# Performance work log

Measured on AMD Instinct MI355X. Metric: run time of the kernel, lower is better.

Reference implementation:

```python
import jax, jax.numpy as jnp
import numpy as np

DIM = 256
L = 16            # block_size (query rows per leaf block)
H = 8             # num_heads
D = DIM // H      # head_dim = 32
KC = L + 1        # key count: L leaf nodes + 1 block (mean) node, layout '16x17'
B = 2
N = 32768         # multiple of L -> no padding path
NB = N // L       # 2048 blocks
SCALE = D ** -0.5


def setup_inputs() -> dict:
    key = jax.random.key(0)
    ks = jax.random.split(key, 8)
    x = jax.random.normal(ks[0], (B, N, DIM), jnp.float32)
    attn_mask = jax.random.randint(ks[1], (NB, L, KC), 0, 2, dtype=jnp.int32)
    ar = jnp.arange(L)
    attn_mask = attn_mask.at[:, ar, ar].set(1)  # self always visible -> no all-masked rows
    edge_feats = jax.random.normal(ks[2], (NB, L, KC, 4), jnp.float32)
    s = DIM ** -0.5
    Wqkv = jax.random.normal(ks[3], (3 * DIM, DIM), jnp.float32) * s
    bqkv = jnp.zeros((3 * DIM,), jnp.float32)
    Wproj = jax.random.normal(ks[4], (DIM, DIM), jnp.float32) * s
    bproj = jnp.zeros((DIM,), jnp.float32)
    Wgate = jax.random.normal(ks[5], (H, 4), jnp.float32) * 0.01  # nn.init.normal_(std=0.01)
    bgate = jnp.zeros((H,), jnp.float32)
    return {"x": x, "attn_mask": attn_mask, "edge_feats": edge_feats,
            "Wqkv": Wqkv, "bqkv": bqkv, "Wproj": Wproj, "bproj": bproj,
            "Wgate": Wgate, "bgate": bgate}


def reference(x, attn_mask, edge_feats, Wqkv, bqkv, Wproj, bproj, Wgate, bgate):
    # x: [B, N, C] -> blocks [B, NB, L, C]
    x_blk = x.reshape(B, NB, L, DIM)
    block_node = x_blk.mean(axis=2, keepdims=True)           # virtual block node
    kv = jnp.concatenate([x_blk, block_node], axis=2)         # [B, NB, KC, C]

    # qkv projections (slice of the fused Linear; rows are independent so math is identical)
    q = x_blk @ Wqkv[:DIM].T + bqkv[:DIM]
    k = kv @ Wqkv[DIM:2 * DIM].T + bqkv[DIM:2 * DIM]
    v = kv @ Wqkv[2 * DIM:].T + bqkv[2 * DIM:]
    q = q.reshape(B, NB, L, H, D)
    k = k.reshape(B, NB, KC, H, D)
    v = v.reshape(B, NB, KC, H, D)

    scores = jnp.einsum('bnqhd,bnkhd->bnqkh', q, k) * SCALE   # [B, NB, L, KC, H]

    # physics bias: zero out + set channel 3 = 1 for block node column and self (diagonal)
    ar = jnp.arange(L)
    unit = jnp.array([0.0, 0.0, 0.0, 1.0], edge_feats.dtype)
    bias = edge_feats.at[:, :, L, :].set(unit)                # block-node column
    bias = bias.at[:, ar, ar, :].set(unit)                    # self bias on diagonal
    bias = jnp.broadcast_to(bias[None], (B, NB, L, KC, 4))    # expand over batch

    scores = scores + bias[..., 3:4]

    mask0 = (attn_mask[None] == 0)[..., None]                 # [1, NB, L, KC, 1]
    scores = jnp.where(mask0, -jnp.inf, scores)
    attn = jax.nn.softmax(scores, axis=3)

    gate = jnp.einsum('bnqkf,hf->bnqkh', bias, Wgate) + bgate  # edge-conditioned gate
    gate = jnp.where(mask0, 0.0, gate)

    combined = attn + gate
    out = jnp.einsum('bnqkh,bnkhd->bnqhd', combined, v).reshape(B, N, DIM)
    return out @ Wproj.T + bproj
```

## Files before the change

### kernel.cpp

```cpp
#include <hip/hip_runtime.h>
#include <cstdint>
#include <cstddef>

#define B_SZ 2
#define N_SEQ 32768
#define NB 2048
#define HD 32
#define LQ 16
#define KCNT 17
#define M_ROWS 65536
#define SCALE_F 0.17677669529663687f

typedef __attribute__((ext_vector_type(8))) short sv8;
typedef __attribute__((ext_vector_type(4))) short sv4;
typedef __attribute__((ext_vector_type(4))) float f4;

__device__ __forceinline__ short f2bf(float f) {
  unsigned u = __builtin_bit_cast(unsigned, f);
  u = (u + 0x7FFFu + ((u >> 16) & 1u)) >> 16;
  return (short)u;
}
__device__ __forceinline__ float bf2f(short s) {
  unsigned u = ((unsigned)(unsigned short)s) << 16;
  return __builtin_bit_cast(float, u);
}
__device__ __forceinline__ void gload16(const void* g, void* l) {
  __builtin_amdgcn_global_load_lds(
      (const __attribute__((address_space(1))) unsigned int*)g,
      (__attribute__((address_space(3))) unsigned int*)l, 16, 0, 0);
}
__device__ __forceinline__ f4 mfma16(sv8 a, sv8 b, f4 c) {
  return __builtin_amdgcn_mfma_f32_16x16x32_bf16(a, b, c, 0, 0, 0);
}

__global__ __launch_bounds__(256) void split256(const float* __restrict__ src,
                                                short* __restrict__ dst, int n4) {
  int i = blockIdx.x * 256 + threadIdx.x;
  if (i >= n4) return;
  float4 v = ((const float4*)src)[i];
  size_t row = (size_t)(i >> 6);
  int c = (i & 63) * 4;
  float fv[4] = {v.x, v.y, v.z, v.w};
  sv4 hi, lo;
#pragma unroll
  for (int j = 0; j < 4; ++j) {
    short h = f2bf(fv[j]);
    hi[j] = h;
    lo[j] = f2bf(fv[j] - bf2f(h));
  }
  *(sv4*)&dst[row * 512 + c] = hi;
  *(sv4*)&dst[row * 512 + 256 + c] = lo;
}

__global__ __launch_bounds__(256) void cast256(const float* __restrict__ src,
                                               short* __restrict__ dst, int n4) {
  int i = blockIdx.x * 256 + threadIdx.x;
  if (i >= n4) return;
  float4 v = ((const float4*)src)[i];
  sv4 h = {f2bf(v.x), f2bf(v.y), f2bf(v.z), f2bf(v.w)};
  *(sv4*)&dst[(size_t)i * 4] = h;
}

__global__ __launch_bounds__(256) void gemm_bf_qkv(
    const short* __restrict__ A1, const short* __restrict__ B2,
    const float* __restrict__ bias, short* __restrict__ Qbf,
    short* __restrict__ Kbf, short* __restrict__ Vbf) {
  __shared__ __align__(16) short Ahs[2][128][32];
  __shared__ __align__(16) short Bhs[2][128][32];
  const int tid = threadIdx.x;
  const int w = tid >> 6, l = tid & 63;
  const int wm = w >> 1, wn = w & 1;
  const int bid = blockIdx.x;
  const int chunk = (6 * 512) >> 3;
  const int lbid = (bid & 7) * chunk + (bid >> 3);
  const int nti = lbid % 6, mti = lbid / 6;
  const int m0 = mti * 128, n0 = nti * 128;
  const int lr = l >> 2;
  const int lc = (l & 3) * 8;
  const int fr = l & 15, kg = (l >> 4) * 8;
  f4 acc[4][4] = {};
#pragma unroll
  for (int i = 0; i < 2; ++i) {
    const int row = w * 32 + i * 16;
    gload16(A1 + (size_t)(m0 + row + lr) * 256 + lc, (void*)&Ahs[0][row][0]);
    gload16(B2 + (size_t)(n0 + row + lr) * 512 + lc, (void*)&Bhs[0][row][0]);
  }
  asm volatile("s_waitcnt vmcnt(0)" ::: "memory");
  __builtin_amdgcn_s_barrier();
  int cur = 0;
  for (int s = 0; s < 8; ++s) {
    if (s < 7) {
      const int sk = (s + 1) * 32;
#pragma unroll
      for (int i = 0; i < 2; ++i) {
        const int row = w * 32 + i * 16;
        gload16(A1 + (size_t)(m0 + row + lr) * 256 + sk + lc,
                (void*)&Ahs[cur ^ 1][row][0]);
        gload16(B2 + (size_t)(n0 + row + lr) * 512 + sk + lc,
                (void*)&Bhs[cur ^ 1][row][0]);
      }
    }
    if (s > 0) {
      if (s < 7) asm volatile("s_waitcnt vmcnt(4)" ::: "memory");
      else asm volatile("s_waitcnt vmcnt(0)" ::: "memory");
      __builtin_amdgcn_s_barrier();
    }
    sv8 fa[4], fb[4];
#pragma unroll
    for (int t = 0; t < 4; ++t) {
      fa[t] = *(const sv8*)&Ahs[cur][wm * 64 + t * 16 + fr][kg];
      fb[t] = *(const sv8*)&Bhs[cur][wn * 64 + t * 16 + fr][kg];
    }
#pragma unroll
    for (int mt = 0; mt < 4; ++mt)
#pragma unroll
      for (int nt = 0; nt < 4; ++nt)
        acc[mt][nt] = mfma16(fa[mt], fb[nt], acc[mt][nt]);
    asm volatile("s_waitcnt lgkmcnt(0)" ::: "memory");
    __builtin_amdgcn_s_barrier();
    cur ^= 1;
  }
  short* dst = (nti < 2) ? Qbf : ((nti < 4) ? Kbf : Vbf);
  const int r0 = (l >> 4) * 4;
#pragma unroll
  for (int mt = 0; mt < 4; ++mt)
#pragma unroll
    for (int nt = 0; nt < 4; ++nt) {
      const int n = n0 + wn * 64 + nt * 16 + fr;
      const float bv = bias[n];
      const int nn = n & 255;
      const size_t mb = (size_t)(m0 + wm * 64 + mt * 16 + r0);
#pragma unroll
      for (int j = 0; j < 4; ++j)
        dst[(mb + j) * 256 + nn] = f2bf(acc[mt][nt][j] + bv);
    }
}

__global__ __launch_bounds__(256) void gemm_proj1(
    const short* __restrict__ A1, const short* __restrict__ B2,
    const float* __restrict__ bias, float* __restrict__ C) {
  __shared__ __align__(16) short Ahs[2][128][32];
  __shared__ __align__(16) short Bhs[2][128][32];
  const int tid = threadIdx.x;
  const int w = tid >> 6, l = tid & 63;
  const int wm = w >> 1, wn = w & 1;
  const int bid = blockIdx.x;
  const int chunk = (2 * 512) >> 3;
  const int lbid = (bid & 7) * chunk + (bid >> 3);
  const int nti = lbid % 2, mti = lbid / 2;
  const int m0 = mti * 128, n0 = nti * 128;
  const int lr = l >> 2;
  const int lc = (l & 3) * 8;
  const int fr = l & 15, kg = (l >> 4) * 8;
  f4 acc[4][4] = {};
#pragma unroll
  for (int i = 0; i < 2; ++i) {
    const int row = w * 32 + i * 16;
    gload16(A1 + (size_t)(m0 + row + lr) * 256 + lc, (void*)&Ahs[0][row][0]);
    gload16(B2 + (size_t)(n0 + row + lr) * 512 + lc, (void*)&Bhs[0][row][0]);
  }
  asm volatile("s_waitcnt vmcnt(0)" ::: "memory");
  __builtin_amdgcn_s_barrier();
  int cur = 0;
  for (int s = 0; s < 8; ++s) {
    if (s < 7) {
      const int sk = (s + 1) * 32;
#pragma unroll
      for (int i = 0; i < 2; ++i) {
        const int row = w * 32 + i * 16;
        gload16(A1 + (size_t)(m0 + row + lr) * 256 + sk + lc,
                (void*)&Ahs[cur ^ 1][row][0]);
        gload16(B2 + (size_t)(n0 + row + lr) * 512 + sk + lc,
                (void*)&Bhs[cur ^ 1][row][0]);
      }
    }
    if (s > 0) {
      if (s < 7) asm volatile("s_waitcnt vmcnt(4)" ::: "memory");
      else asm volatile("s_waitcnt vmcnt(0)" ::: "memory");
      __builtin_amdgcn_s_barrier();
    }
    sv8 fa[4], fb[4];
#pragma unroll
    for (int t = 0; t < 4; ++t) {
      fa[t] = *(const sv8*)&Ahs[cur][wm * 64 + t * 16 + fr][kg];
      fb[t] = *(const sv8*)&Bhs[cur][wn * 64 + t * 16 + fr][kg];
    }
#pragma unroll
    for (int mt = 0; mt < 4; ++mt)
#pragma unroll
      for (int nt = 0; nt < 4; ++nt)
        acc[mt][nt] = mfma16(fa[mt], fb[nt], acc[mt][nt]);
    asm volatile("s_waitcnt lgkmcnt(0)" ::: "memory");
    __builtin_amdgcn_s_barrier();
    cur ^= 1;
  }
  const int r0 = (l >> 4) * 4;
#pragma unroll
  for (int mt = 0; mt < 4; ++mt)
#pragma unroll
    for (int nt = 0; nt < 4; ++nt) {
      const int n = n0 + wn * 64 + nt * 16 + fr;
      const float bv = bias[n];
      const size_t mb = (size_t)(m0 + wm * 64 + mt * 16 + r0);
#pragma unroll
      for (int j = 0; j < 4; ++j) C[(mb + j) * 256 + n] = acc[mt][nt][j] + bv;
    }
}

__global__ __launch_bounds__(256, 4) void attn_v7(
    const short* __restrict__ Qb, const short* __restrict__ Kb,
    const short* __restrict__ Vb, const int* __restrict__ amask,
    const float* __restrict__ efeat, const float* __restrict__ Wgate,
    const float* __restrict__ bgate, short* __restrict__ AO) {
  __shared__ __align__(16) short Kl[16 * 264];
  __shared__ __align__(16) short Vl[32 * 264];
  __shared__ __align__(16) short Ol[16 * 264];
  __shared__ float4 Es[LQ * KCNT];
  __shared__ int Ms[LQ * KCNT];

  const int tid = threadIdx.x, g = blockIdx.x;
  const int b = g >> 11, nb = g & (NB - 1);
  const size_t tok0 = (size_t)(b * N_SEQ + nb * LQ);
  const int w = tid >> 6, l = tid & 63;
  const int ln = l & 15, lg = l >> 4;
  const f4 fzero = {0.f, 0.f, 0.f, 0.f};

  sv8 qf[2];
#pragma unroll
  for (int hh = 0; hh < 2; ++hh) {
    const int h = w * 2 + hh;
    qf[hh] = *(const sv8*)(Qb + (tok0 + ln) * 256 + h * 32 + lg * 8);
  }

#pragma unroll
  for (int i = 0; i < 2; ++i) {
    const int f = tid + i * 256;
    const int t = f >> 5, c8 = (f & 31) * 8;
    *(sv8*)&Kl[t * 264 + c8] = *(const sv8*)(Kb + (tok0 + t) * 256 + c8);
    *(sv8*)&Vl[t * 264 + c8] = *(const sv8*)(Vb + (tok0 + t) * 256 + c8);
  }
  {
    const sv8 z = {};
    for (int z8 = tid; z8 < 528; z8 += 256) *(sv8*)&Vl[4224 + z8 * 8] = z;
  }
  {
    const float4* esrc = (const float4*)(efeat + (size_t)nb * LQ * KCNT * 4);
    const int* msrc = amask + (size_t)nb * LQ * KCNT;
    Es[tid] = esrc[tid];
    Ms[tid] = msrc[tid];
    if (tid < LQ * KCNT - 256) {
      Es[256 + tid] = esrc[256 + tid];
      Ms[256 + tid] = msrc[256 + tid];
    }
  }
  __syncthreads();

  const int q = ln;
#pragma unroll
  for (int hh = 0; hh < 2; ++hh) {
    const int h = w * 2 + hh;
    sv8 ka = *(const sv8*)&Kl[ln * 264 + h * 32 + lg * 8];
    f4 sr = mfma16(ka, qf[hh], fzero);

    const float wg0 = Wgate[h * 4], wg1 = Wgate[h * 4 + 1];
    const float wg2 = Wgate[h * 4 + 2], wg3 = Wgate[h * 4 + 3];
    const float bg = bgate[h];

    float rs = sr[0] + sr[1] + sr[2] + sr[3];
    rs += __shfl_xor(rs, 16);
    rs += __shfl_xor(rs, 32);

    float s_[4], gt_[4];
    int vis_[4];
#pragma unroll
    for (int j = 0; j < 4; ++j) {
      const int kc = lg * 4 + j;
      float e0, e1, e2, e3;
      if (kc == q) { e0 = e1 = e2 = 0.f; e3 = 1.f; }
      else { float4 e = Es[q * KCNT + kc]; e0 = e.x; e1 = e.y; e2 = e.z; e3 = e.w; }
      const int m = Ms[q * KCNT + kc];
      vis_[j] = m;
      s_[j] = sr[j] * SCALE_F + e3;
      gt_[j] = m ? (e0 * wg0 + e1 * wg1 + e2 * wg2 + e3 * wg3 + bg) : 0.f;
    }
    const int m16 = Ms[q * KCNT + 16];
    const float s16 = rs * 0.0625f * SCALE_F + 1.0f;

    float mx = -1e30f;
#pragma unroll
    for (int j = 0; j < 4; ++j)
      if (vis_[j]) mx = fmaxf(mx, s_[j]);
    mx = fmaxf(mx, __shfl_xor(mx, 16));
    mx = fmaxf(mx, __shfl_xor(mx, 32));
    if (m16) mx = fmaxf(mx, s16);

    float p_[4], den = 0.f;
#pragma unroll
    for (int j = 0; j < 4; ++j) {
      p_[j] = vis_[j] ? __expf(s_[j] - mx) : 0.f;
      den += p_[j];
    }
    den += __shfl_xor(den, 16);
    den += __shfl_xor(den, 32);
    const float p16 = m16 ? __expf(s16 - mx) : 0.f;
    den += p16;
    const float inv = 1.f / den;
    const float gt16 = m16 ? (wg3 + bg) : 0.f;
    const float cb16 = (p16 * inv + gt16) * 0.0625f;
    float pc[4];
#pragma unroll
    for (int j = 0; j < 4; ++j) pc[j] = p_[j] * inv + gt_[j] + cb16;

    sv8 pa;
#pragma unroll
    for (int e = 0; e < 8; ++e) {
      const int kc = lg * 8 + e;
      const int src = ((kc >> 2) << 4) | q;
      const float v0 = __shfl(pc[e & 3], src);
      pa[e] = (kc < 16) ? f2bf(v0) : (short)0;
    }

#pragma unroll
    for (int t = 0; t < 2; ++t) {
      sv8 vb;
#pragma unroll
      for (int e = 0; e < 8; ++e)
        vb[e] = Vl[(lg * 8 + e) * 264 + h * 32 + t * 16 + ln];
      f4 oacc = mfma16(pa, vb, fzero);
#pragma unroll
      for (int j = 0; j < 4; ++j)
        Ol[(lg * 4 + j) * 264 + h * 32 + t * 16 + ln] = f2bf(oacc[j]);
    }
  }
  __syncthreads();

#pragma unroll
  for (int i = 0; i < 2; ++i) {
    const int f = tid + i * 256;
    const int t = f >> 5, c8 = (f & 31) * 8;
    *(sv8*)(AO + (tok0 + t) * 256 + c8) = *(const sv8*)&Ol[t * 264 + c8];
  }
}

extern "C" void kernel_launch(void* const* d_in, const int* in_sizes, int n_in,
                              void* d_out, int out_size, void* d_ws, size_t ws_size,
                              hipStream_t stream) {
  const float* x = (const float*)d_in[0];
  const int* amask = (const int*)d_in[1];
  const float* efeat = (const float*)d_in[2];
  const float* Wqkv = (const float*)d_in[3];
  const float* bqkv = (const float*)d_in[4];
  const float* Wproj = (const float*)d_in[5];
  const float* bproj = (const float*)d_in[6];
  const float* Wgate = (const float*)d_in[7];
  const float* bgate = (const float*)d_in[8];
  float* out = (float*)d_out;

  char* ws = (char*)d_ws;
  const size_t QB_SZ = (size_t)M_ROWS * 256 * 2;
  const size_t W2Q_SZ = (size_t)768 * 512 * 2;
  const size_t W2P_SZ = (size_t)256 * 512 * 2;
  if (ws_size < 5 * QB_SZ + W2Q_SZ + W2P_SZ) return;

  short* X1 = (short*)ws;
  short* Qbf = (short*)(ws + QB_SZ);
  short* Kbf = (short*)(ws + 2 * QB_SZ);
  short* Vbf = (short*)(ws + 3 * QB_SZ);
  short* AOh = (short*)(ws + 4 * QB_SZ);
  short* W2Q = (short*)(ws + 5 * QB_SZ);
  short* W2P = (short*)(ws + 5 * QB_SZ + W2Q_SZ);

  cast256<<<dim3(M_ROWS * 64 / 256), 256, 0, stream>>>(x, X1, M_ROWS * 64);
  split256<<<dim3(768 * 64 / 256), 256, 0, stream>>>(Wqkv, W2Q, 768 * 64);
  split256<<<dim3(256 * 64 / 256), 256, 0, stream>>>(Wproj, W2P, 256 * 64);
  gemm_bf_qkv<<<dim3(6 * 512), 256, 0, stream>>>(X1, W2Q, bqkv, Qbf, Kbf, Vbf);
  attn_v7<<<dim3(B_SZ * NB), 256, 0, stream>>>(Qbf, Kbf, Vbf, amask, efeat,
                                               Wgate, bgate, AOh);
  gemm_proj1<<<dim3(2 * 512), 256, 0, stream>>>(AOh, W2P, bproj, out);
}
```

Baseline: 131.8 us.

## Fuse x bf16 cast into QKV GEMM, merge weight casts, shrink attention LDS

Removes the standalone cast kernel for x: the QKV GEMM now reads fp32 x directly, converts it to bf16 in registers, and writes it to shared memory, with the next tile's loads overlapped with the MFMAs. The two weight split kernels become a single weight cast kernel, and its output uses a 256-wide row stride. Previously the weights were stored with a 512 stride split into hi and lo halves, but the GEMMs only read the first 256 columns, so the lo half was never used. The attention kernel drops the zero-padded upper half of the V tile by wrapping row indices, shrinking LDS and raising the occupancy hint from 4 to 5. Trade-offs: each GEMM tile re-reads x as fp32 (twice the bytes), and the conversion is done once per N tile, six times per row.

```diff
diff --git a/kernel.cpp b/kernel.cpp
--- a/kernel.cpp
+++ b/kernel.cpp
@@ -33,36 +33,23 @@
   return __builtin_amdgcn_mfma_f32_16x16x32_bf16(a, b, c, 0, 0, 0);
 }
 
-__global__ __launch_bounds__(256) void split256(const float* __restrict__ src,
-                                                short* __restrict__ dst, int n4) {
-  int i = blockIdx.x * 256 + threadIdx.x;
-  if (i >= n4) return;
-  float4 v = ((const float4*)src)[i];
-  size_t row = (size_t)(i >> 6);
-  int c = (i & 63) * 4;
-  float fv[4] = {v.x, v.y, v.z, v.w};
-  sv4 hi, lo;
-#pragma unroll
-  for (int j = 0; j < 4; ++j) {
-    short h = f2bf(fv[j]);
-    hi[j] = h;
-    lo[j] = f2bf(fv[j] - bf2f(h));
-  }
-  *(sv4*)&dst[row * 512 + c] = hi;
-  *(sv4*)&dst[row * 512 + 256 + c] = lo;
-}
-
-__global__ __launch_bounds__(256) void cast256(const float* __restrict__ src,
-                                               short* __restrict__ dst, int n4) {
-  int i = blockIdx.x * 256 + threadIdx.x;
-  if (i >= n4) return;
-  float4 v = ((const float4*)src)[i];
+__global__ __launch_bounds__(256) void cast_w(
+    const float* __restrict__ wq, const float* __restrict__ wp,
+    short* __restrict__ W1, short* __restrict__ WP1) {
+  const int i = blockIdx.x * 256 + threadIdx.x;
+  const float* src;
+  short* dst;
+  int off;
+  if (i < 49152) { src = wq; dst = W1; off = i; }
+  else if (i < 49152 + 16384) { src = wp; dst = WP1; off = i - 49152; }
+  else return;
+  float4 v = ((const float4*)src)[off];
   sv4 h = {f2bf(v.x), f2bf(v.y), f2bf(v.z), f2bf(v.w)};
-  *(sv4*)&dst[(size_t)i * 4] = h;
-}
-
-__global__ __launch_bounds__(256) void gemm_bf_qkv(
-    const short* __restrict__ A1, const short* __restrict__ B2,
+  *(sv4*)&dst[(size_t)off * 4] = h;
+}
+
+__global__ __launch_bounds__(256) void gemm_fused_qkv(
+    const float* __restrict__ Xf, const short* __restrict__ B1,
     const float* __restrict__ bias, short* __restrict__ Qbf,
     short* __restrict__ Kbf, short* __restrict__ Vbf) {
   __shared__ __align__(16) short Ahs[2][128][32];
@@ -71,73 +58,92 @@
   const int w = tid >> 6, l = tid & 63;
   const int wm = w >> 1, wn = w & 1;
   const int bid = blockIdx.x;
-  const int chunk = (6 * 512) >> 3;
-  const int lbid = (bid & 7) * chunk + (bid >> 3);
+  const int chunkc = (6 * 512) >> 3;
+  const int lbid = (bid & 7) * chunkc + (bid >> 3);
   const int nti = lbid % 6, mti = lbid / 6;
   const int m0 = mti * 128, n0 = nti * 128;
-  const int lr = l >> 2;
-  const int lc = (l & 3) * 8;
+  const int lr = l >> 2, lc = (l & 3) * 8;
   const int fr = l & 15, kg = (l >> 4) * 8;
+  const int ar = w * 32 + lr, ac = lc;
   f4 acc[4][4] = {};
+
+#pragma unroll
+  for (int i = 0; i < 2; ++i)
+    gload16(B1 + (size_t)(n0 + w * 32 + i * 16 + lr) * 256 + lc,
+            (void*)&Bhs[0][w * 32 + i * 16][0]);
 #pragma unroll
   for (int i = 0; i < 2; ++i) {
-    const int row = w * 32 + i * 16;
-    gload16(A1 + (size_t)(m0 + row + lr) * 256 + lc, (void*)&Ahs[0][row][0]);
-    gload16(B2 + (size_t)(n0 + row + lr) * 512 + lc, (void*)&Bhs[0][row][0]);
-  }
-  asm volatile("s_waitcnt vmcnt(0)" ::: "memory");
+    const float* ap = Xf + (size_t)(m0 + ar + i * 16) * 256 + ac;
+    float4 x0 = *(const float4*)ap;
+    float4 x1 = *(const float4*)(ap + 4);
+    sv8 o;
+    o[0] = f2bf(x0.x); o[1] = f2bf(x0.y); o[2] = f2bf(x0.z); o[3] = f2bf(x0.w);
+    o[4] = f2bf(x1.x); o[5] = f2bf(x1.y); o[6] = f2bf(x1.z); o[7] = f2bf(x1.w);
+    *(sv8*)&Ahs[0][ar + i * 16][ac] = o;
+  }
+  asm volatile("s_waitcnt vmcnt(0) lgkmcnt(0)" ::: "memory");
   __builtin_amdgcn_s_barrier();
-  int cur = 0;
+
   for (int s = 0; s < 8; ++s) {
+    const int cb = s & 1, nbuf = cb ^ 1;
+    float4 pa0[2], pa1[2];
     if (s < 7) {
       const int sk = (s + 1) * 32;
 #pragma unroll
+      for (int i = 0; i < 2; ++i)
+        gload16(B1 + (size_t)(n0 + w * 32 + i * 16 + lr) * 256 + sk + lc,
+                (void*)&Bhs[nbuf][w * 32 + i * 16][0]);
+#pragma unroll
       for (int i = 0; i < 2; ++i) {
-        const int row = w * 32 + i * 16;
-        gload16(A1 + (size_t)(m0 + row + lr) * 256 + sk + lc,
-                (void*)&Ahs[cur ^ 1][row][0]);
-        gload16(B2 + (size_t)(n0 + row + lr) * 512 + sk + lc,
-                (void*)&Bhs[cur ^ 1][row][0]);
+        const float* ap = Xf + (size_t)(m0 + ar + i * 16) * 256 + sk + ac;
+        pa0[i] = *(const float4*)ap;
+        pa1[i] = *(const float4*)(ap + 4);
       }
     }
-    if (s > 0) {
-      if (s < 7) asm volatile("s_waitcnt vmcnt(4)" ::: "memory");
-      else asm volatile("s_waitcnt vmcnt(0)" ::: "memory");
-      __builtin_amdgcn_s_barrier();
-    }
     sv8 fa[4], fb[4];
 #pragma unroll
     for (int t = 0; t < 4; ++t) {
-      fa[t] = *(const sv8*)&Ahs[cur][wm * 64 + t * 16 + fr][kg];
-      fb[t] = *(const sv8*)&Bhs[cur][wn * 64 + t * 16 + fr][kg];
+      fa[t] = *(const sv8*)&Ahs[cb][wm * 64 + t * 16 + fr][kg];
+      fb[t] = *(const sv8*)&Bhs[cb][wn * 64 + t * 16 + fr][kg];
     }
 #pragma unroll
     for (int mt = 0; mt < 4; ++mt)
 #pragma unroll
-      for (int nt = 0; nt < 4; ++nt)
-        acc[mt][nt] = mfma16(fa[mt], fb[nt], acc[mt][nt]);
-    asm volatile("s_waitcnt lgkmcnt(0)" ::: "memory");
+      for (int nt2 = 0; nt2 < 4; ++nt2)
+        acc[mt][nt2] = mfma16(fa[mt], fb[nt2], acc[mt][nt2]);
+    if (s < 7) {
+#pragma unroll
+      for (int i = 0; i < 2; ++i) {
+        sv8 o;
+        o[0] = f2bf(pa0[i].x); o[1] = f2bf(pa0[i].y);
+        o[2] = f2bf(pa0[i].z); o[3] = f2bf(pa0[i].w);
+        o[4] = f2bf(pa1[i].x); o[5] = f2bf(pa1[i].y);
+        o[6] = f2bf(pa1[i].z); o[7] = f2bf(pa1[i].w);
+        *(sv8*)&Ahs[nbuf][ar + i * 16][ac] = o;
+      }
+    }
+    asm volatile("s_waitcnt vmcnt(0) lgkmcnt(0)" ::: "memory");
     __builtin_amdgcn_s_barrier();
-    cur ^= 1;
-  }
+  }
+
   short* dst = (nti < 2) ? Qbf : ((nti < 4) ? Kbf : Vbf);
   const int r0 = (l >> 4) * 4;
 #pragma unroll
   for (int mt = 0; mt < 4; ++mt)
 #pragma unroll
-    for (int nt = 0; nt < 4; ++nt) {
-      const int n = n0 + wn * 64 + nt * 16 + fr;
+    for (int nt2 = 0; nt2 < 4; ++nt2) {
+      const int n = n0 + wn * 64 + nt2 * 16 + fr;
       const float bv = bias[n];
       const int nn = n & 255;
       const size_t mb = (size_t)(m0 + wm * 64 + mt * 16 + r0);
 #pragma unroll
       for (int j = 0; j < 4; ++j)
-        dst[(mb + j) * 256 + nn] = f2bf(acc[mt][nt][j] + bv);
+        dst[(mb + j) * 256 + nn] = f2bf(acc[mt][nt2][j] + bv);
     }
 }
 
 __global__ __launch_bounds__(256) void gemm_proj1(
-    const short* __restrict__ A1, const short* __restrict__ B2,
+    const short* __restrict__ A1, const short* __restrict__ B1,
     const float* __restrict__ bias, float* __restrict__ C) {
   __shared__ __align__(16) short Ahs[2][128][32];
   __shared__ __align__(16) short Bhs[2][128][32];
@@ -145,19 +151,18 @@
   const int w = tid >> 6, l = tid & 63;
   const int wm = w >> 1, wn = w & 1;
   const int bid = blockIdx.x;
-  const int chunk = (2 * 512) >> 3;
-  const int lbid = (bid & 7) * chunk + (bid >> 3);
+  const int chunkc = (2 * 512) >> 3;
+  const int lbid = (bid & 7) * chunkc + (bid >> 3);
   const int nti = lbid % 2, mti = lbid / 2;
   const int m0 = mti * 128, n0 = nti * 128;
-  const int lr = l >> 2;
-  const int lc = (l & 3) * 8;
+  const int lr = l >> 2, lc = (l & 3) * 8;
   const int fr = l & 15, kg = (l >> 4) * 8;
   f4 acc[4][4] = {};
 #pragma unroll
   for (int i = 0; i < 2; ++i) {
     const int row = w * 32 + i * 16;
     gload16(A1 + (size_t)(m0 + row + lr) * 256 + lc, (void*)&Ahs[0][row][0]);
-    gload16(B2 + (size_t)(n0 + row + lr) * 512 + lc, (void*)&Bhs[0][row][0]);
+    gload16(B1 + (size_t)(n0 + row + lr) * 256 + lc, (void*)&Bhs[0][row][0]);
   }
   asm volatile("s_waitcnt vmcnt(0)" ::: "memory");
   __builtin_amdgcn_s_barrier();
@@ -170,7 +175,7 @@
         const int row = w * 32 + i * 16;
         gload16(A1 + (size_t)(m0 + row + lr) * 256 + sk + lc,
                 (void*)&Ahs[cur ^ 1][row][0]);
-        gload16(B2 + (size_t)(n0 + row + lr) * 512 + sk + lc,
+        gload16(B1 + (size_t)(n0 + row + lr) * 256 + sk + lc,
                 (void*)&Bhs[cur ^ 1][row][0]);
       }
     }
@@ -188,8 +193,8 @@
 #pragma unroll
     for (int mt = 0; mt < 4; ++mt)
 #pragma unroll
-      for (int nt = 0; nt < 4; ++nt)
-        acc[mt][nt] = mfma16(fa[mt], fb[nt], acc[mt][nt]);
+      for (int nt2 = 0; nt2 < 4; ++nt2)
+        acc[mt][nt2] = mfma16(fa[mt], fb[nt2], acc[mt][nt2]);
     asm volatile("s_waitcnt lgkmcnt(0)" ::: "memory");
     __builtin_amdgcn_s_barrier();
     cur ^= 1;
@@ -198,22 +203,22 @@
 #pragma unroll
   for (int mt = 0; mt < 4; ++mt)
 #pragma unroll
-    for (int nt = 0; nt < 4; ++nt) {
-      const int n = n0 + wn * 64 + nt * 16 + fr;
+    for (int nt2 = 0; nt2 < 4; ++nt2) {
+      const int n = n0 + wn * 64 + nt2 * 16 + fr;
       const float bv = bias[n];
       const size_t mb = (size_t)(m0 + wm * 64 + mt * 16 + r0);
 #pragma unroll
-      for (int j = 0; j < 4; ++j) C[(mb + j) * 256 + n] = acc[mt][nt][j] + bv;
-    }
-}
-
-__global__ __launch_bounds__(256, 4) void attn_v7(
+      for (int j = 0; j < 4; ++j) C[(mb + j) * 256 + n] = acc[mt][nt2][j] + bv;
+    }
+}
+
+__global__ __launch_bounds__(256, 5) void attn_v7(
     const short* __restrict__ Qb, const short* __restrict__ Kb,
     const short* __restrict__ Vb, const int* __restrict__ amask,
     const float* __restrict__ efeat, const float* __restrict__ Wgate,
     const float* __restrict__ bgate, short* __restrict__ AO) {
   __shared__ __align__(16) short Kl[16 * 264];
-  __shared__ __align__(16) short Vl[32 * 264];
+  __shared__ __align__(16) short Vl[16 * 264];
   __shared__ __align__(16) short Ol[16 * 264];
   __shared__ float4 Es[LQ * KCNT];
   __shared__ int Ms[LQ * KCNT];
@@ -238,10 +243,6 @@
     const int t = f >> 5, c8 = (f & 31) * 8;
     *(sv8*)&Kl[t * 264 + c8] = *(const sv8*)(Kb + (tok0 + t) * 256 + c8);
     *(sv8*)&Vl[t * 264 + c8] = *(const sv8*)(Vb + (tok0 + t) * 256 + c8);
-  }
-  {
-    const sv8 z = {};
-    for (int z8 = tid; z8 < 528; z8 += 256) *(sv8*)&Vl[4224 + z8 * 8] = z;
   }
   {
     const float4* esrc = (const float4*)(efeat + (size_t)nb * LQ * KCNT * 4);
@@ -324,8 +325,10 @@
     for (int t = 0; t < 2; ++t) {
       sv8 vb;
 #pragma unroll
-      for (int e = 0; e < 8; ++e)
-        vb[e] = Vl[(lg * 8 + e) * 264 + h * 32 + t * 16 + ln];
+      for (int e = 0; e < 8; ++e) {
+        const int vr = (lg * 8 + e) & 15;
+        vb[e] = Vl[vr * 264 + h * 32 + t * 16 + ln];
+      }
       f4 oacc = mfma16(pa, vb, fzero);
 #pragma unroll
       for (int j = 0; j < 4; ++j)
@@ -358,23 +361,21 @@
 
   char* ws = (char*)d_ws;
   const size_t QB_SZ = (size_t)M_ROWS * 256 * 2;
-  const size_t W2Q_SZ = (size_t)768 * 512 * 2;
-  const size_t W2P_SZ = (size_t)256 * 512 * 2;
-  if (ws_size < 5 * QB_SZ + W2Q_SZ + W2P_SZ) return;
-
-  short* X1 = (short*)ws;
-  short* Qbf = (short*)(ws + QB_SZ);
-  short* Kbf = (short*)(ws + 2 * QB_SZ);
-  short* Vbf = (short*)(ws + 3 * QB_SZ);
-  short* AOh = (short*)(ws + 4 * QB_SZ);
-  short* W2Q = (short*)(ws + 5 * QB_SZ);
-  short* W2P = (short*)(ws + 5 * QB_SZ + W2Q_SZ);
-
-  cast256<<<dim3(M_ROWS * 64 / 256), 256, 0, stream>>>(x, X1, M_ROWS * 64);
-  split256<<<dim3(768 * 64 / 256), 256, 0, stream>>>(Wqkv, W2Q, 768 * 64);
-  split256<<<dim3(256 * 64 / 256), 256, 0, stream>>>(Wproj, W2P, 256 * 64);
-  gemm_bf_qkv<<<dim3(6 * 512), 256, 0, stream>>>(X1, W2Q, bqkv, Qbf, Kbf, Vbf);
+  const size_t W1_SZ = (size_t)768 * 256 * 2;
+  const size_t WP1_SZ = (size_t)256 * 256 * 2;
+  if (ws_size < 4 * QB_SZ + W1_SZ + WP1_SZ) return;
+
+  short* Qbf = (short*)ws;
+  short* Kbf = (short*)(ws + QB_SZ);
+  short* Vbf = (short*)(ws + 2 * QB_SZ);
+  short* AOh = (short*)(ws + 3 * QB_SZ);
+  short* W1 = (short*)(ws + 4 * QB_SZ);
+  short* WP1 = (short*)(ws + 4 * QB_SZ + W1_SZ);
+
+  cast_w<<<dim3((49152 + 16384 + 255) / 256), 256, 0, stream>>>(Wqkv, Wproj,
+                                                                W1, WP1);
+  gemm_fused_qkv<<<dim3(6 * 512), 256, 0, stream>>>(x, W1, bqkv, Qbf, Kbf, Vbf);
   attn_v7<<<dim3(B_SZ * NB), 256, 0, stream>>>(Qbf, Kbf, Vbf, amask, efeat,
                                                Wgate, bgate, AOh);
-  gemm_proj1<<<dim3(2 * 512), 256, 0, stream>>>(AOh, W2P, bproj, out);
-}
+  gemm_proj1<<<dim3(2 * 512), 256, 0, stream>>>(AOh, WP1, bproj, out);
+}
```

Measured after the change: 138.5 us. 1.05x slower.
